# Kernel tuning notes

Measured on AMD Instinct MI355X. Metric: run time of the kernel, lower is better.

Reference implementation:

```python
import jax, jax.numpy as jnp
import numpy as np

DIM = 768
N_HEADS = 12
HEAD_DIM = DIM // N_HEADS
B, T = 2, 2048


def setup_inputs() -> dict:
    key = jax.random.key(0)
    ks = jax.random.split(key, 11)
    s = 0.02
    return {
        "q_in": jax.random.normal(ks[0], (B, T, DIM), jnp.float32),
        "k_in": jax.random.normal(ks[1], (B, T, DIM), jnp.float32),
        "v_in": jax.random.normal(ks[2], (B, T, DIM), jnp.float32),
        "Wq": jax.random.normal(ks[3], (DIM, DIM), jnp.float32) * s,
        "bq": jnp.zeros((DIM,), jnp.float32),
        "Wk": jax.random.normal(ks[4], (DIM, DIM), jnp.float32) * s,
        "bk": jnp.zeros((DIM,), jnp.float32),
        "Wv": jax.random.normal(ks[5], (DIM, DIM), jnp.float32) * s,
        "bv": jnp.zeros((DIM,), jnp.float32),
        "Wo": jax.random.normal(ks[6], (DIM, DIM), jnp.float32) * s,
        "bo": jnp.zeros((DIM,), jnp.float32),
    }


def reference(q_in, k_in, v_in, Wq, bq, Wk, bk, Wv, bv, Wo, bo):
    b, t, c = q_in.shape
    scale = HEAD_DIM ** -0.5
    # linear projections (torch Linear: x @ W.T + b)
    q = q_in @ Wq.T + bq
    k = k_in @ Wk.T + bk
    v = v_in @ Wv.T + bv
    # [b, t, h, d] -> [b, h, t, d]
    q = q.reshape(b, t, N_HEADS, HEAD_DIM).transpose(0, 2, 1, 3)
    k = k.reshape(b, t, N_HEADS, HEAD_DIM).transpose(0, 2, 1, 3)
    v = v.reshape(b, t, N_HEADS, HEAD_DIM).transpose(0, 2, 1, 3)
    scores = jnp.einsum("bhqd,bhkd->bhqk", q, k) * scale  # full TxT scores
    probs = jax.nn.softmax(scores, axis=-1)
    attn = jnp.einsum("bhqk,bhkd->bhqd", probs, v)
    attn = attn.transpose(0, 2, 1, 3).reshape(b, t, c)
    return attn @ Wo.T + bo
```

## Files before the change

### kernel.cpp

```cpp
#include <hip/hip_runtime.h>


typedef unsigned short u16;
typedef __attribute__((ext_vector_type(8))) short short8;
typedef __attribute__((ext_vector_type(4))) float float4v;

#define DIMC 768
#define NTOK 4096
#define NHD  12
#define HDD  64
#define SEQT 2048

__device__ __forceinline__ u16 f2bf(float f) {
  union { float f; unsigned u; } v; v.f = f;
  unsigned r = v.u + 0x7fffu + ((v.u >> 16) & 1u);
  return (u16)(r >> 16);
}
__device__ __forceinline__ float bf2f(u16 u) {
  union { unsigned u; float f; } v; v.u = ((unsigned)u) << 16;
  return v.f;
}

__global__ __launch_bounds__(256) void cvt3_kernel(
    const float* __restrict__ a, const float* __restrict__ b, const float* __restrict__ c,
    u16* __restrict__ oa, u16* __restrict__ ob, u16* __restrict__ oc) {
  int z = blockIdx.y;
  const float* s = (z == 0) ? a : (z == 1) ? b : c;
  u16* d = (z == 0) ? oa : (z == 1) ? ob : oc;
  size_t i = ((size_t)blockIdx.x * 256 + threadIdx.x) * 4;
  float4 v = *(const float4*)(s + i);
  *(ushort4*)(d + i) = make_ushort4(f2bf(v.x), f2bf(v.y), f2bf(v.z), f2bf(v.w));
}

__global__ __launch_bounds__(256) void cvt4_kernel(
    const float* __restrict__ a, const float* __restrict__ b,
    const float* __restrict__ c, const float* __restrict__ e,
    u16* __restrict__ oa, u16* __restrict__ ob, u16* __restrict__ oc, u16* __restrict__ oe) {
  int z = blockIdx.y;
  const float* s = (z == 0) ? a : (z == 1) ? b : (z == 2) ? c : e;
  u16* d = (z == 0) ? oa : (z == 1) ? ob : (z == 2) ? oc : oe;
  size_t i = ((size_t)blockIdx.x * 256 + threadIdx.x) * 4;
  float4 v = *(const float4*)(s + i);
  *(ushort4*)(d + i) = make_ushort4(f2bf(v.x), f2bf(v.y), f2bf(v.z), f2bf(v.w));
}

__device__ __forceinline__ void gemm_mainloop2(
    const u16* __restrict__ X, const u16* __restrict__ W,
    int m0, int n0, u16* Als, u16* Bls, float4v acc[4][2]) {
  int tid = threadIdx.x;
  int sr = tid >> 3, sc = (tid & 7) * 8;
  int w = tid >> 6, lane = tid & 63, quad = lane >> 4, r15 = lane & 15;
  int wm = (w >> 1) * 64, wn = (w & 1) * 32;
  const u16* xp0 = X + (size_t)(m0 + sr) * DIMC + sc;
  const u16* xp1 = xp0 + 32 * DIMC;
  const u16* xp2 = xp0 + 64 * DIMC;
  const u16* xp3 = xp0 + 96 * DIMC;
  const u16* wp0 = W + (size_t)(n0 + sr) * DIMC + sc;
  const u16* wp1 = wp0 + 32 * DIMC;
  uint4 pa0 = *(const uint4*)xp0, pa1 = *(const uint4*)xp1;
  uint4 pa2 = *(const uint4*)xp2, pa3 = *(const uint4*)xp3;
  uint4 pb0 = *(const uint4*)wp0, pb1 = *(const uint4*)wp1;
  for (int k0 = 0; k0 < DIMC; k0 += 64) {
    __syncthreads();
    *(uint4*)(Als + sr * 72 + sc) = pa0;
    *(uint4*)(Als + (sr + 32) * 72 + sc) = pa1;
    *(uint4*)(Als + (sr + 64) * 72 + sc) = pa2;
    *(uint4*)(Als + (sr + 96) * 72 + sc) = pa3;
    *(uint4*)(Bls + sr * 72 + sc) = pb0;
    *(uint4*)(Bls + (sr + 32) * 72 + sc) = pb1;
    __syncthreads();
    int kn = k0 + 64;
    if (kn < DIMC) {
      pa0 = *(const uint4*)(xp0 + kn); pa1 = *(const uint4*)(xp1 + kn);
      pa2 = *(const uint4*)(xp2 + kn); pa3 = *(const uint4*)(xp3 + kn);
      pb0 = *(const uint4*)(wp0 + kn); pb1 = *(const uint4*)(wp1 + kn);
    }
    #pragma unroll
    for (int sk = 0; sk < 2; sk++) {
      short8 af[4], bf[2];
      #pragma unroll
      for (int mf = 0; mf < 4; mf++)
        af[mf] = *(const short8*)(Als + (wm + mf * 16 + r15) * 72 + sk * 32 + quad * 8);
      #pragma unroll
      for (int nf = 0; nf < 2; nf++)
        bf[nf] = *(const short8*)(Bls + (wn + nf * 16 + r15) * 72 + sk * 32 + quad * 8);
      #pragma unroll
      for (int mf = 0; mf < 4; mf++)
        #pragma unroll
        for (int nf = 0; nf < 2; nf++)
          acc[mf][nf] = __builtin_amdgcn_mfma_f32_16x16x32_bf16(af[mf], bf[nf], acc[mf][nf], 0, 0, 0);
    }
  }
}

__global__ __launch_bounds__(256, 4) void gemm_qkv(
    const u16* __restrict__ xq, const u16* __restrict__ xk, const u16* __restrict__ xv,
    const u16* __restrict__ wq, const u16* __restrict__ wk, const u16* __restrict__ wv,
    const float* __restrict__ bq, const float* __restrict__ bk, const float* __restrict__ bv,
    u16* __restrict__ Qh, u16* __restrict__ Kh, u16* __restrict__ Vt) {
  __shared__ __align__(16) u16 Als[128 * 72];
  __shared__ __align__(16) u16 Bls[64 * 72];
  int z = blockIdx.z;
  const u16* X = (z == 0) ? xq : (z == 1) ? xk : xv;
  const u16* W = (z == 0) ? wq : (z == 1) ? wk : wv;
  const float* bias = (z == 0) ? bq : (z == 1) ? bk : bv;
  int m0 = blockIdx.x * 128, n0 = blockIdx.y * 64;
  float4v acc[4][2];
  #pragma unroll
  for (int i = 0; i < 4; i++)
    #pragma unroll
    for (int j = 0; j < 2; j++)
      #pragma unroll
      for (int r = 0; r < 4; r++) acc[i][j][r] = 0.f;
  gemm_mainloop2(X, W, m0, n0, Als, Bls, acc);
  int tid = threadIdx.x, w = tid >> 6, lane = tid & 63, quad = lane >> 4, r15 = lane & 15;
  int wm = (w >> 1) * 64, wn = (w & 1) * 32;
  if (z == 2) {
    __syncthreads();
    u16* T = Als;
    #pragma unroll
    for (int mf = 0; mf < 4; mf++)
      #pragma unroll
      for (int nf = 0; nf < 2; nf++)
        #pragma unroll
        for (int rg = 0; rg < 4; rg++) {
          int mloc = wm + mf * 16 + quad * 4 + rg;
          int nloc = wn + nf * 16 + r15;
          T[nloc * 136 + mloc] = f2bf(acc[mf][nf][rg] + bias[n0 + nloc]);
        }
    __syncthreads();
    int d = tid >> 2, seg = tid & 3;
    int b = m0 >> 11, t0 = m0 & 2047, h = n0 >> 6;
    size_t base = (((size_t)(b * NHD + h)) * HDD + d) * SEQT + t0 + seg * 32;
    const u16* src = T + d * 136 + seg * 32;
    #pragma unroll
    for (int j = 0; j < 4; j++)
      *(uint4*)(Vt + base + j * 8) = *(const uint4*)(src + j * 8);
  } else {
    #pragma unroll
    for (int mf = 0; mf < 4; mf++)
      #pragma unroll
      for (int nf = 0; nf < 2; nf++)
        #pragma unroll
        for (int rg = 0; rg < 4; rg++) {
          int m = m0 + wm + mf * 16 + quad * 4 + rg;
          int n = n0 + wn + nf * 16 + r15;
          float val = acc[mf][nf][rg] + bias[n];
          if (z == 0) val *= 0.180336880f;
          int b = m >> 11, t = m & 2047, h = n >> 6, d = n & 63;
          u16 o = f2bf(val);
          size_t bh = (size_t)(b * NHD + h);
          if (z == 0) Qh[(bh * SEQT + t) * HDD + d] = o;
          else Kh[(bh * SEQT + t) * HDD + d] = o;
        }
  }
}

__global__ __launch_bounds__(256, 4) void attn_kernel(
    const u16* __restrict__ Qh, const u16* __restrict__ Kh, const u16* __restrict__ Vt,
    u16* __restrict__ Opart, float* __restrict__ Lpart) {
  __shared__ __align__(16) u16 Kls[64 * 72];
  __shared__ __align__(16) u16 Vls[64 * 72];
  __shared__ __align__(16) u16 Pls[4 * 32 * 72];
  int bh = blockIdx.y, sp = blockIdx.z, qt0 = blockIdx.x * 128;
  int tid = threadIdx.x, w = tid >> 6, lane = tid & 63, quad = lane >> 4, r15 = lane & 15;
  int qw = qt0 + w * 32;
  int tile0 = (sp < 2) ? sp * 11 : 22;
  int nt = (sp < 2) ? 11 : 10;
  int kt0 = tile0 * 64;

  short8 qa[2][2];
  #pragma unroll
  for (int qs = 0; qs < 2; qs++) {
    const u16* qp = Qh + ((size_t)bh * SEQT + qw + qs * 16 + r15) * HDD + quad * 8;
    qa[qs][0] = *(const short8*)qp;
    qa[qs][1] = *(const short8*)(qp + 32);
  }
  short8 ones;
  #pragma unroll
  for (int i = 0; i < 8; i++) ones[i] = (short)0x3F80;
  float4v fzero;
  #pragma unroll
  for (int r = 0; r < 4; r++) fzero[r] = 0.f;

  float4v oacc[2][4], lacc[2];
  #pragma unroll
  for (int qs = 0; qs < 2; qs++) {
    #pragma unroll
    for (int r = 0; r < 4; r++) lacc[qs][r] = 0.f;
    #pragma unroll
    for (int dt = 0; dt < 4; dt++)
      #pragma unroll
      for (int r = 0; r < 4; r++) oacc[qs][dt][r] = 0.f;
  }

  const u16* Kbase = Kh + (size_t)bh * SEQT * HDD;
  const u16* Vbase = Vt + (size_t)bh * HDD * SEQT;
  u16* Pw = Pls + w * (32 * 72);
  int sr = tid >> 3, sc = (tid & 7) * 8;

  uint4 pk0 = *(const uint4*)(Kbase + (size_t)(kt0 + sr) * HDD + sc);
  uint4 pk1 = *(const uint4*)(Kbase + (size_t)(kt0 + sr + 32) * HDD + sc);
  uint4 pv0 = *(const uint4*)(Vbase + (size_t)sr * SEQT + kt0 + sc);
  uint4 pv1 = *(const uint4*)(Vbase + (size_t)(sr + 32) * SEQT + kt0 + sc);

  for (int it = 0; it < nt; it++) {
    __syncthreads();
    *(uint4*)(Kls + sr * 72 + sc) = pk0;
    *(uint4*)(Kls + (sr + 32) * 72 + sc) = pk1;
    *(uint4*)(Vls + sr * 72 + sc) = pv0;
    *(uint4*)(Vls + (sr + 32) * 72 + sc) = pv1;
    __syncthreads();
    int nit = it + 1; if (nit == nt) nit = 0;
    int ktn = kt0 + nit * 64;
    pk0 = *(const uint4*)(Kbase + (size_t)(ktn + sr) * HDD + sc);
    pk1 = *(const uint4*)(Kbase + (size_t)(ktn + sr + 32) * HDD + sc);
    pv0 = *(const uint4*)(Vbase + (size_t)sr * SEQT + ktn + sc);
    pv1 = *(const uint4*)(Vbase + (size_t)(sr + 32) * SEQT + ktn + sc);

    float4v st[4][2];
    #pragma unroll
    for (int nk = 0; nk < 4; nk++) {
      short8 k0 = *(const short8*)(Kls + (nk * 16 + r15) * 72 + quad * 8);
      short8 k1 = *(const short8*)(Kls + (nk * 16 + r15) * 72 + 32 + quad * 8);
      #pragma unroll
      for (int qs = 0; qs < 2; qs++) {
        float4v z = __builtin_amdgcn_mfma_f32_16x16x32_bf16(k0, qa[qs][0], fzero, 0, 0, 0);
        z = __builtin_amdgcn_mfma_f32_16x16x32_bf16(k1, qa[qs][1], z, 0, 0, 0);
        st[nk][qs] = z;
      }
    }
    #pragma unroll
    for (int qs = 0; qs < 2; qs++)
      #pragma unroll
      for (int nk = 0; nk < 4; nk++) {
        float p0 = __builtin_amdgcn_exp2f(st[nk][qs][0]);
        float p1 = __builtin_amdgcn_exp2f(st[nk][qs][1]);
        float p2 = __builtin_amdgcn_exp2f(st[nk][qs][2]);
        float p3 = __builtin_amdgcn_exp2f(st[nk][qs][3]);
        unsigned lo = __builtin_amdgcn_perm(__float_as_uint(p1), __float_as_uint(p0), 0x07060302u);
        unsigned hi = __builtin_amdgcn_perm(__float_as_uint(p3), __float_as_uint(p2), 0x07060302u);
        *(uint2*)(Pw + (qs * 16 + r15) * 72 + nk * 16 + quad * 4) = make_uint2(lo, hi);
      }
    short8 pa[2][2];
    #pragma unroll
    for (int qs = 0; qs < 2; qs++) {
      pa[qs][0] = *(const short8*)(Pw + (qs * 16 + r15) * 72 + quad * 8);
      pa[qs][1] = *(const short8*)(Pw + (qs * 16 + r15) * 72 + 32 + quad * 8);
      lacc[qs] = __builtin_amdgcn_mfma_f32_16x16x32_bf16(pa[qs][0], ones, lacc[qs], 0, 0, 0);
      lacc[qs] = __builtin_amdgcn_mfma_f32_16x16x32_bf16(pa[qs][1], ones, lacc[qs], 0, 0, 0);
    }
    #pragma unroll
    for (int dt = 0; dt < 4; dt++) {
      short8 v0 = *(const short8*)(Vls + (dt * 16 + r15) * 72 + quad * 8);
      short8 v1 = *(const short8*)(Vls + (dt * 16 + r15) * 72 + 32 + quad * 8);
      #pragma unroll
      for (int qs = 0; qs < 2; qs++) {
        oacc[qs][dt] = __builtin_amdgcn_mfma_f32_16x16x32_bf16(pa[qs][0], v0, oacc[qs][dt], 0, 0, 0);
        oacc[qs][dt] = __builtin_amdgcn_mfma_f32_16x16x32_bf16(pa[qs][1], v1, oacc[qs][dt], 0, 0, 0);
      }
    }
  }
  size_t obase = ((size_t)sp * 2 * NHD + bh) * SEQT;
  #pragma unroll
  for (int qs = 0; qs < 2; qs++)
    #pragma unroll
    for (int rg = 0; rg < 4; rg++) {
      int q = qw + qs * 16 + quad * 4 + rg;
      u16* orow = Opart + (obase + q) * HDD;
      #pragma unroll
      for (int dt = 0; dt < 4; dt++) orow[dt * 16 + r15] = f2bf(oacc[qs][dt][rg]);
      if (r15 == 0) Lpart[obase + q] = lacc[qs][rg];
    }
}

__global__ __launch_bounds__(256) void merge_kernel(
    const u16* __restrict__ Opart, const float* __restrict__ Lpart, u16* __restrict__ X2) {
  const size_t NXe = (size_t)2 * NHD * SEQT * HDD;
  const size_t LS = (size_t)2 * NHD * SEQT;
  int tid = threadIdx.x;
  int row = blockIdx.x * 32 + (tid >> 3);
  int dcol = (tid & 7) * 8;
  int bh = row >> 11, t = row & 2047;
  size_t off = (size_t)row * HDD + dcol;
  float inv = 1.0f / (Lpart[row] + Lpart[row + LS] + Lpart[row + 2 * LS]);
  int b = bh / NHD, h = bh % NHD;
  u16 o[8];
  #pragma unroll
  for (int half = 0; half < 2; half++) {
    ushort4 a = *(const ushort4*)(Opart + off + half * 4);
    ushort4 c = *(const ushort4*)(Opart + off + NXe + half * 4);
    ushort4 e = *(const ushort4*)(Opart + off + 2 * NXe + half * 4);
    o[half * 4 + 0] = f2bf((bf2f(a.x) + bf2f(c.x) + bf2f(e.x)) * inv);
    o[half * 4 + 1] = f2bf((bf2f(a.y) + bf2f(c.y) + bf2f(e.y)) * inv);
    o[half * 4 + 2] = f2bf((bf2f(a.z) + bf2f(c.z) + bf2f(e.z)) * inv);
    o[half * 4 + 3] = f2bf((bf2f(a.w) + bf2f(c.w) + bf2f(e.w)) * inv);
  }
  *(uint4*)(X2 + ((size_t)b * SEQT + t) * DIMC + h * HDD + dcol) = *(uint4*)o;
}

__global__ __launch_bounds__(256, 4) void gemm_out(
    const u16* __restrict__ X2, const u16* __restrict__ wo,
    const float* __restrict__ bo, float* __restrict__ out) {
  __shared__ __align__(16) u16 Als[128 * 72];
  __shared__ __align__(16) u16 Bls[64 * 72];
  int m0 = blockIdx.x * 128, n0 = blockIdx.y * 64;
  float4v acc[4][2];
  #pragma unroll
  for (int i = 0; i < 4; i++)
    #pragma unroll
    for (int j = 0; j < 2; j++)
      #pragma unroll
      for (int r = 0; r < 4; r++) acc[i][j][r] = 0.f;
  gemm_mainloop2(X2, wo, m0, n0, Als, Bls, acc);
  int tid = threadIdx.x, w = tid >> 6, lane = tid & 63, quad = lane >> 4, r15 = lane & 15;
  int wm = (w >> 1) * 64, wn = (w & 1) * 32;
  #pragma unroll
  for (int mf = 0; mf < 4; mf++)
    #pragma unroll
    for (int nf = 0; nf < 2; nf++)
      #pragma unroll
      for (int rg = 0; rg < 4; rg++) {
        int m = m0 + wm + mf * 16 + quad * 4 + rg;
        int n = n0 + wn + nf * 16 + r15;
        out[(size_t)m * DIMC + n] = acc[mf][nf][rg] + bo[n];
      }
}

extern "C" void kernel_launch(void* const* d_in, const int* in_sizes, int n_in,
                              void* d_out, int out_size, void* d_ws, size_t ws_size,
                              hipStream_t stream) {
  const float* q_in = (const float*)d_in[0];
  const float* k_in = (const float*)d_in[1];
  const float* v_in = (const float*)d_in[2];
  const float* Wq = (const float*)d_in[3];
  const float* bq = (const float*)d_in[4];
  const float* Wk = (const float*)d_in[5];
  const float* bk = (const float*)d_in[6];
  const float* Wv = (const float*)d_in[7];
  const float* bv = (const float*)d_in[8];
  const float* Wo = (const float*)d_in[9];
  const float* bo = (const float*)d_in[10];

  const size_t NX = (size_t)NTOK * DIMC;
  const size_t NW = (size_t)DIMC * DIMC;
  u16* ws = (u16*)d_ws;
  u16* qb = ws;
  u16* kb = qb + NX;
  u16* vb = kb + NX;
  u16* wqb = vb + NX;
  u16* wkb = wqb + NW;
  u16* wvb = wkb + NW;
  u16* wob = wvb + NW;
  u16* Qh = wob + NW;
  u16* Kh = Qh + NX;
  u16* Vt = Kh + NX;
  u16* X2 = Vt + NX;
  u16* Opart = qb;
  float* Lpart = (float*)wqb;

  cvt3_kernel<<<dim3(NX / 1024, 3), 256, 0, stream>>>(q_in, k_in, v_in, qb, kb, vb);
  cvt4_kernel<<<dim3(NW / 1024, 4), 256, 0, stream>>>(Wq, Wk, Wv, Wo, wqb, wkb, wvb, wob);
  gemm_qkv<<<dim3(NTOK / 128, DIMC / 64, 3), 256, 0, stream>>>(
      qb, kb, vb, wqb, wkb, wvb, bq, bk, bv, Qh, Kh, Vt);
  attn_kernel<<<dim3(SEQT / 128, 2 * NHD, 3), 256, 0, stream>>>(Qh, Kh, Vt, Opart, Lpart);
  merge_kernel<<<dim3(2 * NHD * SEQT / 32), 256, 0, stream>>>(Opart, Lpart, X2);
  gemm_out<<<dim3(NTOK / 128, DIMC / 64), 256, 0, stream>>>(X2, wob, bo, (float*)d_out);
}
```

Measured before the change: 190.9 us.

## Swizzle attention LDS tiles, add MFMA priority hints, merge conversion kernels

Replaces the padded 72-wide LDS rows for K, V and P with unpadded 64-wide rows using an XOR swizzle to avoid bank conflicts, cutting shared memory per block. The occupancy hint rises from 4 to 5 blocks per CU to use the freed LDS. s_setprio brackets the MFMA sections so waves doing matrix math get issue priority. The two fp32-to-bf16 conversion kernels become one launch, removing a kernel launch. The swizzle indexing adds a few integer ops and must stay consistent between writers and readers.

```diff
diff --git a/kernel.cpp b/kernel.cpp
--- a/kernel.cpp
+++ b/kernel.cpp
@@ -21,25 +21,25 @@
   return v.f;
 }
 
-__global__ __launch_bounds__(256) void cvt3_kernel(
-    const float* __restrict__ a, const float* __restrict__ b, const float* __restrict__ c,
-    u16* __restrict__ oa, u16* __restrict__ ob, u16* __restrict__ oc) {
-  int z = blockIdx.y;
-  const float* s = (z == 0) ? a : (z == 1) ? b : c;
-  u16* d = (z == 0) ? oa : (z == 1) ? ob : oc;
-  size_t i = ((size_t)blockIdx.x * 256 + threadIdx.x) * 4;
-  float4 v = *(const float4*)(s + i);
-  *(ushort4*)(d + i) = make_ushort4(f2bf(v.x), f2bf(v.y), f2bf(v.z), f2bf(v.w));
-}
-
-__global__ __launch_bounds__(256) void cvt4_kernel(
-    const float* __restrict__ a, const float* __restrict__ b,
-    const float* __restrict__ c, const float* __restrict__ e,
-    u16* __restrict__ oa, u16* __restrict__ ob, u16* __restrict__ oc, u16* __restrict__ oe) {
-  int z = blockIdx.y;
-  const float* s = (z == 0) ? a : (z == 1) ? b : (z == 2) ? c : e;
-  u16* d = (z == 0) ? oa : (z == 1) ? ob : (z == 2) ? oc : oe;
-  size_t i = ((size_t)blockIdx.x * 256 + threadIdx.x) * 4;
+__global__ __launch_bounds__(256) void cvt_all(
+    const float* __restrict__ a0, const float* __restrict__ a1, const float* __restrict__ a2,
+    const float* __restrict__ a3, const float* __restrict__ a4, const float* __restrict__ a5,
+    const float* __restrict__ a6,
+    u16* __restrict__ o0, u16* __restrict__ o1, u16* __restrict__ o2,
+    u16* __restrict__ o3, u16* __restrict__ o4, u16* __restrict__ o5,
+    u16* __restrict__ o6) {
+  int bid = blockIdx.x;
+  const float* s; u16* d; int inner;
+  if (bid < 9216) {
+    int z = bid / 3072; inner = bid - z * 3072;
+    s = (z == 0) ? a0 : (z == 1) ? a1 : a2;
+    d = (z == 0) ? o0 : (z == 1) ? o1 : o2;
+  } else {
+    int r = bid - 9216; int z = r / 576; inner = r - z * 576;
+    s = (z == 0) ? a3 : (z == 1) ? a4 : (z == 2) ? a5 : a6;
+    d = (z == 0) ? o3 : (z == 1) ? o4 : (z == 2) ? o5 : o6;
+  }
+  size_t i = ((size_t)inner * 256 + threadIdx.x) * 4;
   float4 v = *(const float4*)(s + i);
   *(ushort4*)(d + i) = make_ushort4(f2bf(v.x), f2bf(v.y), f2bf(v.z), f2bf(v.w));
 }
@@ -156,12 +156,12 @@
   }
 }
 
-__global__ __launch_bounds__(256, 4) void attn_kernel(
+__global__ __launch_bounds__(256, 5) void attn_kernel(
     const u16* __restrict__ Qh, const u16* __restrict__ Kh, const u16* __restrict__ Vt,
     u16* __restrict__ Opart, float* __restrict__ Lpart) {
-  __shared__ __align__(16) u16 Kls[64 * 72];
-  __shared__ __align__(16) u16 Vls[64 * 72];
-  __shared__ __align__(16) u16 Pls[4 * 32 * 72];
+  __shared__ __align__(16) u16 Kls[64 * 64];
+  __shared__ __align__(16) u16 Vls[64 * 64];
+  __shared__ __align__(16) u16 Pls[4 * 32 * 64];
   int bh = blockIdx.y, sp = blockIdx.z, qt0 = blockIdx.x * 128;
   int tid = threadIdx.x, w = tid >> 6, lane = tid & 63, quad = lane >> 4, r15 = lane & 15;
   int qw = qt0 + w * 32;
@@ -169,6 +169,10 @@
   int nt = (sp < 2) ? 11 : 10;
   int kt0 = tile0 * 64;
 
+  int rr = r15 & 7;
+  int sx0 = (quad ^ rr) * 8;
+  int sx1 = ((4 + quad) ^ rr) * 8;
+
   short8 qa[2][2];
   #pragma unroll
   for (int qs = 0; qs < 2; qs++) {
@@ -196,8 +200,9 @@
 
   const u16* Kbase = Kh + (size_t)bh * SEQT * HDD;
   const u16* Vbase = Vt + (size_t)bh * HDD * SEQT;
-  u16* Pw = Pls + w * (32 * 72);
+  u16* Pw = Pls + w * (32 * 64);
   int sr = tid >> 3, sc = (tid & 7) * 8;
+  int sg = (((tid & 7) ^ (sr & 7)) * 8);
 
   uint4 pk0 = *(const uint4*)(Kbase + (size_t)(kt0 + sr) * HDD + sc);
   uint4 pk1 = *(const uint4*)(Kbase + (size_t)(kt0 + sr + 32) * HDD + sc);
@@ -206,10 +211,10 @@
 
   for (int it = 0; it < nt; it++) {
     __syncthreads();
-    *(uint4*)(Kls + sr * 72 + sc) = pk0;
-    *(uint4*)(Kls + (sr + 32) * 72 + sc) = pk1;
-    *(uint4*)(Vls + sr * 72 + sc) = pv0;
-    *(uint4*)(Vls + (sr + 32) * 72 + sc) = pv1;
+    *(uint4*)(Kls + sr * 64 + sg) = pk0;
+    *(uint4*)(Kls + (sr + 32) * 64 + sg) = pk1;
+    *(uint4*)(Vls + sr * 64 + sg) = pv0;
+    *(uint4*)(Vls + (sr + 32) * 64 + sg) = pv1;
     __syncthreads();
     int nit = it + 1; if (nit == nt) nit = 0;
     int ktn = kt0 + nit * 64;
@@ -219,10 +224,11 @@
     pv1 = *(const uint4*)(Vbase + (size_t)(sr + 32) * SEQT + ktn + sc);
 
     float4v st[4][2];
+    __builtin_amdgcn_s_setprio(1);
     #pragma unroll
     for (int nk = 0; nk < 4; nk++) {
-      short8 k0 = *(const short8*)(Kls + (nk * 16 + r15) * 72 + quad * 8);
-      short8 k1 = *(const short8*)(Kls + (nk * 16 + r15) * 72 + 32 + quad * 8);
+      short8 k0 = *(const short8*)(Kls + (nk * 16 + r15) * 64 + sx0);
+      short8 k1 = *(const short8*)(Kls + (nk * 16 + r15) * 64 + sx1);
       #pragma unroll
       for (int qs = 0; qs < 2; qs++) {
         float4v z = __builtin_amdgcn_mfma_f32_16x16x32_bf16(k0, qa[qs][0], fzero, 0, 0, 0);
@@ -230,6 +236,7 @@
         st[nk][qs] = z;
       }
     }
+    __builtin_amdgcn_s_setprio(0);
     #pragma unroll
     for (int qs = 0; qs < 2; qs++)
       #pragma unroll
@@ -240,26 +247,29 @@
         float p3 = __builtin_amdgcn_exp2f(st[nk][qs][3]);
         unsigned lo = __builtin_amdgcn_perm(__float_as_uint(p1), __float_as_uint(p0), 0x07060302u);
         unsigned hi = __builtin_amdgcn_perm(__float_as_uint(p3), __float_as_uint(p2), 0x07060302u);
-        *(uint2*)(Pw + (qs * 16 + r15) * 72 + nk * 16 + quad * 4) = make_uint2(lo, hi);
+        *(uint2*)(Pw + (qs * 16 + r15) * 64 + (((nk * 4 + quad) ^ (rr << 1)) << 2)) =
+            make_uint2(lo, hi);
       }
     short8 pa[2][2];
+    __builtin_amdgcn_s_setprio(1);
     #pragma unroll
     for (int qs = 0; qs < 2; qs++) {
-      pa[qs][0] = *(const short8*)(Pw + (qs * 16 + r15) * 72 + quad * 8);
-      pa[qs][1] = *(const short8*)(Pw + (qs * 16 + r15) * 72 + 32 + quad * 8);
+      pa[qs][0] = *(const short8*)(Pw + (qs * 16 + r15) * 64 + sx0);
+      pa[qs][1] = *(const short8*)(Pw + (qs * 16 + r15) * 64 + sx1);
       lacc[qs] = __builtin_amdgcn_mfma_f32_16x16x32_bf16(pa[qs][0], ones, lacc[qs], 0, 0, 0);
       lacc[qs] = __builtin_amdgcn_mfma_f32_16x16x32_bf16(pa[qs][1], ones, lacc[qs], 0, 0, 0);
     }
     #pragma unroll
     for (int dt = 0; dt < 4; dt++) {
-      short8 v0 = *(const short8*)(Vls + (dt * 16 + r15) * 72 + quad * 8);
-      short8 v1 = *(const short8*)(Vls + (dt * 16 + r15) * 72 + 32 + quad * 8);
+      short8 v0 = *(const short8*)(Vls + (dt * 16 + r15) * 64 + sx0);
+      short8 v1 = *(const short8*)(Vls + (dt * 16 + r15) * 64 + sx1);
       #pragma unroll
       for (int qs = 0; qs < 2; qs++) {
         oacc[qs][dt] = __builtin_amdgcn_mfma_f32_16x16x32_bf16(pa[qs][0], v0, oacc[qs][dt], 0, 0, 0);
         oacc[qs][dt] = __builtin_amdgcn_mfma_f32_16x16x32_bf16(pa[qs][1], v1, oacc[qs][dt], 0, 0, 0);
       }
     }
+    __builtin_amdgcn_s_setprio(0);
   }
   size_t obase = ((size_t)sp * 2 * NHD + bh) * SEQT;
   #pragma unroll
@@ -359,8 +369,8 @@
   u16* Opart = qb;
   float* Lpart = (float*)wqb;
 
-  cvt3_kernel<<<dim3(NX / 1024, 3), 256, 0, stream>>>(q_in, k_in, v_in, qb, kb, vb);
-  cvt4_kernel<<<dim3(NW / 1024, 4), 256, 0, stream>>>(Wq, Wk, Wv, Wo, wqb, wkb, wvb, wob);
+  cvt_all<<<dim3(11520), 256, 0, stream>>>(
+      q_in, k_in, v_in, Wq, Wk, Wv, Wo, qb, kb, vb, wqb, wkb, wvb, wob);
   gemm_qkv<<<dim3(NTOK / 128, DIMC / 64, 3), 256, 0, stream>>>(
       qb, kb, vb, wqb, wkb, wvb, bq, bk, bv, Qh, Kh, Vt);
   attn_kernel<<<dim3(SEQT / 128, 2 * NHD, 3), 256, 0, stream>>>(Qh, Kh, Vt, Opart, Lpart);
```

Result: slower. 326.3 us (+70.9%).
